# Kernel optimization log

Measured on AMD Instinct MI355X. Metric: run time of the kernel, lower is better.

## Reference

```python
import jax, jax.numpy as jnp
import numpy as np

N_EMBD = 1024
HEADS = 16
HEAD_DIM = N_EMBD // HEADS


def setup_inputs() -> dict:
    key = jax.random.key(0)
    k1, k2 = jax.random.split(key)
    x = jax.random.normal(k1, (2, 2048, N_EMBD), dtype=jnp.float32)
    W_qkv = jax.random.normal(k2, (N_EMBD, 3 * N_EMBD), dtype=jnp.float32) * (N_EMBD ** -0.5)
    b_qkv = jnp.zeros((3 * N_EMBD,), dtype=jnp.float32)
    return {"x": x, "W_qkv": W_qkv, "b_qkv": b_qkv}


def reference(x, W_qkv, b_qkv):
    B, T, _ = x.shape
    qkv = x @ W_qkv + b_qkv                      # [B, T, 3*n_embd]
    q, k, v = jnp.split(qkv, 3, axis=-1)
    q = q.reshape(B, T, HEADS, HEAD_DIM)
    k = k.reshape(B, T, HEADS, HEAD_DIM)
    v = v.reshape(B, T, HEADS, HEAD_DIM)
    attn = jnp.einsum('bthd,bThd->bhtT', q, k) / jnp.sqrt(jnp.float32(HEAD_DIM))
    causal = jnp.tril(jnp.ones((T, T), dtype=bool))  # [T, T]
    attn = jnp.where(causal, attn, -jnp.inf)
    attn = jax.nn.softmax(attn, axis=-1)
    # dropout is identity in deterministic/eval mode (training=False)
    out = jnp.einsum('bhtT,bThd->bthd', attn, v).reshape(B, T, N_EMBD)
    return out
```

## Files before the change

kernel.cpp:

```cpp
#include <hip/hip_runtime.h>
#include <hip/hip_bf16.h>

#define BATCH 2
#define TSEQ  2048
#define NEMBD 1024
#define HEADS 16
#define HDIM  64

typedef short          bf16x8 __attribute__((ext_vector_type(8)));
typedef float          f32x4  __attribute__((ext_vector_type(4)));
typedef unsigned short u16;

__device__ __forceinline__ u16 f2bf(float f) {
  unsigned int u = __float_as_uint(f);
  u += 0x7fffu + ((u >> 16) & 1u);
  return (u16)(u >> 16);
}

__device__ __forceinline__ void gld16(const u16* g, u16* l) {
  __builtin_amdgcn_global_load_lds(
      (const __attribute__((address_space(1))) unsigned int*)g,
      (__attribute__((address_space(3))) unsigned int*)l, 16, 0, 0);
}

__global__ __launch_bounds__(256) void k_prep(const float* __restrict__ x,
                                              u16* __restrict__ xb,
                                              const float* __restrict__ w,
                                              u16* __restrict__ wt) {
  __shared__ float tile[32][33];
  const int b = blockIdx.x;
  const int t = threadIdx.x;
  if (b < 4096) {
    int i = b * 256 + t;
    float4 v = ((const float4*)x)[i];
    ushort4 o;
    o.x = f2bf(v.x); o.y = f2bf(v.y); o.z = f2bf(v.z); o.w = f2bf(v.w);
    ((ushort4*)xb)[i] = o;
  } else {
    const int bt = b - 4096;
    const int n0 = (bt >> 5) * 32;
    const int k0 = (bt & 31) * 32;
    const int r  = t >> 3;
    const int c4 = (t & 7) * 4;
    float4 v = *(const float4*)(w + (size_t)(k0 + r) * 3072 + n0 + c4);
    tile[r][c4 + 0] = v.x; tile[r][c4 + 1] = v.y;
    tile[r][c4 + 2] = v.z; tile[r][c4 + 3] = v.w;
    __syncthreads();
    ushort4 o;
    o.x = f2bf(tile[c4 + 0][r]);
    o.y = f2bf(tile[c4 + 1][r]);
    o.z = f2bf(tile[c4 + 2][r]);
    o.w = f2bf(tile[c4 + 3][r]);
    *(ushort4*)(wt + (size_t)(n0 + r) * 1024 + k0 + c4) = o;
  }
}

__global__ __launch_bounds__(256, 3) void k_qkv_gemm(
    const u16* __restrict__ xb, const u16* __restrict__ wt,
    const float* __restrict__ bias,
    u16* __restrict__ qb, u16* __restrict__ kbuf, u16* __restrict__ vt) {
  __shared__ __align__(16) u16 As[128 * 64];
  __shared__ __align__(16) u16 Bs[128 * 64];

  const int t    = threadIdx.x;
  const int wv   = t >> 6;
  const int lane = t & 63;
  const int m    = lane & 15;
  const int quad = lane >> 4;
  const int lin  = blockIdx.x;
  const int cp   = lin >> 5;
  const int rp   = ((lin & 7) << 2) | ((lin >> 3) & 3);
  const int row0 = rp * 128;
  const int col0 = cp * 128;
  const int wr   = (wv >> 1) * 64;
  const int wc   = (wv & 1) * 64;

  const int sr = wv * 32 + (lane >> 3);
  const int gs = (lane & 7) ^ (sr & 7);
  const u16* ag = xb + (size_t)(row0 + sr) * 1024 + gs * 8;
  const u16* bg = wt + (size_t)(col0 + sr) * 1024 + gs * 8;
  u16* al = As + (wv * 32) * 64;
  u16* bl = Bs + (wv * 32) * 64;

  f32x4 acc[4][4];
  const f32x4 zf = {0.f, 0.f, 0.f, 0.f};
  for (int i = 0; i < 4; ++i)
    for (int j = 0; j < 4; ++j) acc[i][j] = zf;

  for (int kt = 0; kt < 16; ++kt) {
    const int kk = kt * 64;
    __syncthreads();
    gld16(ag + kk,             al);
    gld16(ag + kk +  8 * 1024, al +  8 * 64);
    gld16(ag + kk + 16 * 1024, al + 16 * 64);
    gld16(ag + kk + 24 * 1024, al + 24 * 64);
    gld16(bg + kk,             bl);
    gld16(bg + kk +  8 * 1024, bl +  8 * 64);
    gld16(bg + kk + 16 * 1024, bl + 16 * 64);
    gld16(bg + kk + 24 * 1024, bl + 24 * 64);
    __syncthreads();

#pragma unroll
    for (int h = 0; h < 2; ++h) {
      const int g = ((quad + 4 * h) ^ (m & 7)) * 8;
      bf16x8 af[4], bfr[4];
#pragma unroll
      for (int mt = 0; mt < 4; ++mt)
        af[mt] = *(const bf16x8*)(As + (wr + mt * 16 + m) * 64 + g);
#pragma unroll
      for (int nt = 0; nt < 4; ++nt)
        bfr[nt] = *(const bf16x8*)(Bs + (wc + nt * 16 + m) * 64 + g);
#pragma unroll
      for (int mt = 0; mt < 4; ++mt)
#pragma unroll
        for (int nt = 0; nt < 4; ++nt)
          acc[mt][nt] = __builtin_amdgcn_mfma_f32_16x16x32_bf16(
              af[mt], bfr[nt], acc[mt][nt], 0, 0, 0);
    }
  }

  const int sec = col0 >> 10;
#pragma unroll
  for (int nt = 0; nt < 4; ++nt) {
    const int Cc = col0 + wc + nt * 16 + m;
    const float bv = bias[Cc];
    const int c = Cc & 1023;
    const int h = c >> 6;
    const int d = c & 63;
#pragma unroll
    for (int mt = 0; mt < 4; ++mt) {
      const int Rbase = row0 + wr + mt * 16 + quad * 4;
      const int bb = Rbase >> 11;
      const int t0 = Rbase & 2047;
      const int bh = bb * HEADS + h;
      if (sec == 0) {
#pragma unroll
        for (int rg = 0; rg < 4; ++rg) {
          float v = (acc[mt][nt][rg] + bv) * 0.125f;
          qb[(size_t)(bh * TSEQ + t0 + rg) * HDIM + d] = f2bf(v);
        }
      } else if (sec == 1) {
#pragma unroll
        for (int rg = 0; rg < 4; ++rg) {
          float v = acc[mt][nt][rg] + bv;
          kbuf[(size_t)(bh * TSEQ + t0 + rg) * HDIM + d] = f2bf(v);
        }
      } else {
        ushort4 pk;
        pk.x = f2bf(acc[mt][nt][0] + bv);
        pk.y = f2bf(acc[mt][nt][1] + bv);
        pk.z = f2bf(acc[mt][nt][2] + bv);
        pk.w = f2bf(acc[mt][nt][3] + bv);
        *(ushort4*)(vt + (size_t)(bh * HDIM + d) * TSEQ + t0) = pk;
      }
    }
  }
}

__global__ __launch_bounds__(256, 3) void k_attn(
    const u16* __restrict__ qb, const u16* __restrict__ kbuf,
    const u16* __restrict__ vt, float* __restrict__ out) {
  __shared__ __align__(16) u16 Kb[2][4096];
  __shared__ __align__(16) u16 Vb[2][4096];
  __shared__ __align__(16) u16 pt[4][16 * 72];

  const int t     = threadIdx.x;
  const int wv    = t >> 6;
  const int lane  = t & 63;
  const int m     = lane & 15;
  const int quad  = lane >> 4;
  const int bh    = blockIdx.x & 31;
  const int qtg   = 31 - (blockIdx.x >> 5);
  const int qbase = (qtg * 4 + wv) * 16;
  const int nkt   = qtg + 1;

  u16* pw = &pt[wv][0];

  const u16* qrow = qb + ((size_t)bh * TSEQ + qbase + m) * HDIM + quad * 8;
  bf16x8 aq0 = *(const bf16x8*)(qrow);
  bf16x8 aq1 = *(const bf16x8*)(qrow + 32);

  const int sr = wv * 16 + (lane >> 3);
  const int gs = (lane & 7) ^ (sr & 7);
  const u16* kg = kbuf + ((size_t)bh * TSEQ + sr) * HDIM + gs * 8;
  const u16* vg = vt + ((size_t)bh * HDIM + sr) * TSEQ + gs * 8;
  u16* klds = &Kb[0][wv * 16 * 64];
  u16* vlds = &Vb[0][wv * 16 * 64];

  const int swL = (quad ^ (m & 7)) * 8;
  const int swH = ((quad + 4) ^ (m & 7)) * 8;

  f32x4 o[4];
  const f32x4 zf = {0.f, 0.f, 0.f, 0.f};
  for (int nt = 0; nt < 4; ++nt) o[nt] = zf;
  float rsum = 0.f;
  const int qi = qbase + m;

  gld16(kg,             klds);
  gld16(kg + 8 * HDIM,  klds + 8 * 64);
  gld16(vg,             vlds);
  gld16(vg + 8 * TSEQ,  vlds + 8 * 64);
  __syncthreads();

  for (int kt = 0; kt < nkt; ++kt) {
    const int b = kt & 1;
    const u16* kb0 = &Kb[b][0];
    const u16* vb0 = &Vb[b][0];

    f32x4 s[4];
    for (int nt = 0; nt < 4; ++nt) s[nt] = zf;
#pragma unroll
    for (int nt = 0; nt < 4; ++nt) {
      bf16x8 kf = *(const bf16x8*)(kb0 + (nt * 16 + m) * 64 + swL);
      s[nt] = __builtin_amdgcn_mfma_f32_16x16x32_bf16(kf, aq0, s[nt], 0, 0, 0);
    }
#pragma unroll
    for (int nt = 0; nt < 4; ++nt) {
      bf16x8 kf = *(const bf16x8*)(kb0 + (nt * 16 + m) * 64 + swH);
      s[nt] = __builtin_amdgcn_mfma_f32_16x16x32_bf16(kf, aq1, s[nt], 0, 0, 0);
    }

    bf16x8 vfL[4], vfH[4];
#pragma unroll
    for (int nt = 0; nt < 4; ++nt) {
      vfL[nt] = *(const bf16x8*)(vb0 + (nt * 16 + m) * 64 + swL);
      vfH[nt] = *(const bf16x8*)(vb0 + (nt * 16 + m) * 64 + swH);
    }

    if (kt + 1 < nkt) {
      const int nb = (kt + 1) & 1;
      const u16* kgn = kg + (size_t)(kt + 1) * 64 * HDIM;
      const u16* vgn = vg + (kt + 1) * 64;
      u16* kl = &Kb[nb][wv * 16 * 64];
      u16* vl = &Vb[nb][wv * 16 * 64];
      gld16(kgn,            kl);
      gld16(kgn + 8 * HDIM, kl + 8 * 64);
      gld16(vgn,            vl);
      gld16(vgn + 8 * TSEQ, vl + 8 * 64);
    }

    if (kt == nkt - 1) {
      const int kb = kt * 64 + quad * 4;
#pragma unroll
      for (int nt = 0; nt < 4; ++nt)
#pragma unroll
        for (int rg = 0; rg < 4; ++rg)
          if (kb + nt * 16 + rg > qi) s[nt][rg] = -1e30f;
    }

#pragma unroll
    for (int nt = 0; nt < 4; ++nt) {
      float p0 = __expf(s[nt][0]), p1 = __expf(s[nt][1]);
      float p2 = __expf(s[nt][2]), p3 = __expf(s[nt][3]);
      rsum += (p0 + p1) + (p2 + p3);
      ushort4 pk = {f2bf(p0), f2bf(p1), f2bf(p2), f2bf(p3)};
      *(ushort4*)(pw + m * 72 + nt * 16 + quad * 4) = pk;
    }
    bf16x8 bp0 = *(const bf16x8*)(pw + m * 72 + quad * 8);
    bf16x8 bp1 = *(const bf16x8*)(pw + m * 72 + 32 + quad * 8);

#pragma unroll
    for (int nt = 0; nt < 4; ++nt)
      o[nt] = __builtin_amdgcn_mfma_f32_16x16x32_bf16(vfL[nt], bp0, o[nt], 0, 0, 0);
#pragma unroll
    for (int nt = 0; nt < 4; ++nt)
      o[nt] = __builtin_amdgcn_mfma_f32_16x16x32_bf16(vfH[nt], bp1, o[nt], 0, 0, 0);

    __syncthreads();
  }

  rsum += __shfl_xor(rsum, 16);
  rsum += __shfl_xor(rsum, 32);
  const float inv = 1.0f / rsum;

  const int bb = bh >> 4;
  const int h  = bh & 15;
  float* ob = out + ((size_t)(bb * TSEQ + qi) * NEMBD + h * HDIM + quad * 4);
#pragma unroll
  for (int nt = 0; nt < 4; ++nt) {
    float4 st;
    st.x = o[nt][0] * inv; st.y = o[nt][1] * inv;
    st.z = o[nt][2] * inv; st.w = o[nt][3] * inv;
    *(float4*)(ob + nt * 16) = st;
  }
}

extern "C" void kernel_launch(void* const* d_in, const int* in_sizes, int n_in,
                              void* d_out, int out_size, void* d_ws, size_t ws_size,
                              hipStream_t stream) {
  (void)in_sizes; (void)n_in; (void)out_size; (void)ws_size;
  const float* x    = (const float*)d_in[0];
  const float* W    = (const float*)d_in[1];
  const float* bqkv = (const float*)d_in[2];
  float* out = (float*)d_out;

  u16* ws   = (u16*)d_ws;
  u16* qb   = ws;
  u16* kbuf = ws + 4194304;
  u16* vt   = ws + 2 * 4194304;
  u16* xb   = ws + 3 * 4194304;
  u16* wt   = ws + 4 * 4194304;

  hipLaunchKernelGGL(k_prep, dim3(7168), dim3(256), 0, stream, x, xb, W, wt);
  hipLaunchKernelGGL(k_qkv_gemm, dim3(768), dim3(256), 0, stream,
                     xb, wt, bqkv, qb, kbuf, vt);
  hipLaunchKernelGGL(k_attn, dim3(1024), dim3(256), 0, stream,
                     qb, kbuf, vt, out);
}
```

Baseline: 140.5 us.

## Restructure QKV GEMM into double-buffered 256x256 tiles with interleaved loads

The QKV projection GEMM moves from 128x128 tiles with 256 threads to 256x256 tiles with 512 threads. LDS is now double-buffered, and the next k-slice's global-to-LDS loads are split into quarters interleaved with MFMA quadrants, using explicit vmcnt waits, barriers and s_setprio. The goal is to hide load latency behind compute and raise operand reuse per LDS byte. In exchange the grid shrinks to 192 blocks using 128KB of LDS each, which may leave some compute units idle.

```diff
diff --git a/kernel.cpp b/kernel.cpp
--- a/kernel.cpp
+++ b/kernel.cpp
@@ -22,6 +22,9 @@
       (const __attribute__((address_space(1))) unsigned int*)g,
       (__attribute__((address_space(3))) unsigned int*)l, 16, 0, 0);
 }
+
+#define BARSB() do { __builtin_amdgcn_s_barrier();      \
+                     __builtin_amdgcn_sched_barrier(0); } while (0)
 
 __global__ __launch_bounds__(256) void k_prep(const float* __restrict__ x,
                                               u16* __restrict__ xb,
@@ -55,81 +58,145 @@
   }
 }
 
-__global__ __launch_bounds__(256, 3) void k_qkv_gemm(
+__global__ __launch_bounds__(512, 2) void k_qkv_gemm(
     const u16* __restrict__ xb, const u16* __restrict__ wt,
     const float* __restrict__ bias,
     u16* __restrict__ qb, u16* __restrict__ kbuf, u16* __restrict__ vt) {
-  __shared__ __align__(16) u16 As[128 * 64];
-  __shared__ __align__(16) u16 Bs[128 * 64];
+  __shared__ __align__(16) u16 Ab[2][256 * 64];
+  __shared__ __align__(16) u16 Bb[2][256 * 64];
 
   const int t    = threadIdx.x;
-  const int wv   = t >> 6;
+  const int wid  = t >> 6;
   const int lane = t & 63;
   const int m    = lane & 15;
   const int quad = lane >> 4;
-  const int lin  = blockIdx.x;
-  const int cp   = lin >> 5;
-  const int rp   = ((lin & 7) << 2) | ((lin >> 3) & 3);
-  const int row0 = rp * 128;
-  const int col0 = cp * 128;
-  const int wr   = (wv >> 1) * 64;
-  const int wc   = (wv & 1) * 64;
-
-  const int sr = wv * 32 + (lane >> 3);
-  const int gs = (lane & 7) ^ (sr & 7);
-  const u16* ag = xb + (size_t)(row0 + sr) * 1024 + gs * 8;
-  const u16* bg = wt + (size_t)(col0 + sr) * 1024 + gs * 8;
-  u16* al = As + (wv * 32) * 64;
-  u16* bl = Bs + (wv * 32) * 64;
-
-  f32x4 acc[4][4];
+  const int wm   = wid >> 2;
+  const int wn   = wid & 3;
+
+  const int rp   = blockIdx.x & 15;
+  const int cp   = blockIdx.x >> 4;
+  const int row0 = rp * 256;
+  const int col0 = cp * 256;
+
+  const int trA = t >> 3;
+  const int gs  = (t & 7) ^ (trA & 7);
+  const int rB0 = ((t >> 8) & 1) * 64 + (trA & 31);
+  const u16* agp = xb + (size_t)(row0 + trA) * 1024 + gs * 8;
+  const u16* bgp = wt + (size_t)(col0 + rB0) * 1024 + gs * 8;
+  const int ldsArow = wid * 8;
+  const int ldsBrow = (wid >> 2) * 64 + (wid & 3) * 8;
+
+  const int sw0 = (quad ^ (m & 7)) * 8;
+  const int sw1 = ((4 + quad) ^ (m & 7)) * 8;
+
+  f32x4 acc[8][4];
   const f32x4 zf = {0.f, 0.f, 0.f, 0.f};
-  for (int i = 0; i < 4; ++i)
+#pragma unroll
+  for (int i = 0; i < 8; ++i)
+#pragma unroll
     for (int j = 0; j < 4; ++j) acc[i][j] = zf;
 
-  for (int kt = 0; kt < 16; ++kt) {
-    const int kk = kt * 64;
-    __syncthreads();
-    gld16(ag + kk,             al);
-    gld16(ag + kk +  8 * 1024, al +  8 * 64);
-    gld16(ag + kk + 16 * 1024, al + 16 * 64);
-    gld16(ag + kk + 24 * 1024, al + 24 * 64);
-    gld16(bg + kk,             bl);
-    gld16(bg + kk +  8 * 1024, bl +  8 * 64);
-    gld16(bg + kk + 16 * 1024, bl + 16 * 64);
-    gld16(bg + kk + 24 * 1024, bl + 24 * 64);
-    __syncthreads();
-
-#pragma unroll
-    for (int h = 0; h < 2; ++h) {
-      const int g = ((quad + 4 * h) ^ (m & 7)) * 8;
-      bf16x8 af[4], bfr[4];
-#pragma unroll
-      for (int mt = 0; mt < 4; ++mt)
-        af[mt] = *(const bf16x8*)(As + (wr + mt * 16 + m) * 64 + g);
-#pragma unroll
-      for (int nt = 0; nt < 4; ++nt)
-        bfr[nt] = *(const bf16x8*)(Bs + (wc + nt * 16 + m) * 64 + g);
-#pragma unroll
-      for (int mt = 0; mt < 4; ++mt)
-#pragma unroll
-        for (int nt = 0; nt < 4; ++nt)
-          acc[mt][nt] = __builtin_amdgcn_mfma_f32_16x16x32_bf16(
-              af[mt], bfr[nt], acc[mt][nt], 0, 0, 0);
-    }
+  gld16(agp,          &Ab[0][(  0 + ldsArow) * 64]);
+  gld16(agp + 131072, &Ab[0][(128 + ldsArow) * 64]);
+  gld16(agp +  65536, &Ab[0][( 64 + ldsArow) * 64]);
+  gld16(agp + 196608, &Ab[0][(192 + ldsArow) * 64]);
+  gld16(bgp,          &Bb[0][(  0 + ldsBrow) * 64]);
+  gld16(bgp + 131072, &Bb[0][(128 + ldsBrow) * 64]);
+  gld16(bgp +  32768, &Bb[0][( 32 + ldsBrow) * 64]);
+  gld16(bgp + 163840, &Bb[0][(160 + ldsBrow) * 64]);
+  asm volatile("s_waitcnt vmcnt(0)" ::: "memory");
+  BARSB();
+
+  bf16x8 a[4][2], b0[2][2], b1[2][2];
+
+#define RD_A(H)                                                         \
+  _Pragma("unroll") for (int mf = 0; mf < 4; ++mf) {                    \
+    const u16* r_ = cA + (wm * 128 + (H) * 64 + mf * 16 + m) * 64;      \
+    a[mf][0] = *(const bf16x8*)(r_ + sw0);                              \
+    a[mf][1] = *(const bf16x8*)(r_ + sw1);                              \
+  }
+#define RD_B(H, BR)                                                     \
+  _Pragma("unroll") for (int nf = 0; nf < 2; ++nf) {                    \
+    const u16* r_ = cB + (wn * 64 + (H) * 32 + nf * 16 + m) * 64;       \
+    BR[nf][0] = *(const bf16x8*)(r_ + sw0);                             \
+    BR[nf][1] = *(const bf16x8*)(r_ + sw1);                             \
+  }
+#define MFMA_Q(MB, NB, BR)                                              \
+  __builtin_amdgcn_s_setprio(1);                                        \
+  _Pragma("unroll") for (int mf = 0; mf < 4; ++mf)                      \
+    _Pragma("unroll") for (int nf = 0; nf < 2; ++nf) {                  \
+      acc[(MB) + mf][(NB) + nf] = __builtin_amdgcn_mfma_f32_16x16x32_bf16( \
+          a[mf][0], BR[nf][0], acc[(MB) + mf][(NB) + nf], 0, 0, 0);     \
+      acc[(MB) + mf][(NB) + nf] = __builtin_amdgcn_mfma_f32_16x16x32_bf16( \
+          a[mf][1], BR[nf][1], acc[(MB) + mf][(NB) + nf], 0, 0, 0);     \
+    }                                                                   \
+  __builtin_amdgcn_s_setprio(0);
+
+  for (int kt = 0; kt < 15; ++kt) {
+    const u16* cA = &Ab[kt & 1][0];
+    const u16* cB = &Bb[kt & 1][0];
+    u16* nA = &Ab[(kt + 1) & 1][0];
+    u16* nB = &Bb[(kt + 1) & 1][0];
+    const int kn = (kt + 1) * 64;
+
+    RD_A(0)
+    RD_B(0, b0)
+    gld16(agp + kn,          nA + (  0 + ldsArow) * 64);
+    gld16(agp + kn + 131072, nA + (128 + ldsArow) * 64);
+    BARSB();
+    MFMA_Q(0, 0, b0)
+    asm volatile("s_waitcnt vmcnt(2)" ::: "memory");
+    BARSB();
+
+    RD_B(1, b1)
+    gld16(bgp + kn,          nB + (  0 + ldsBrow) * 64);
+    gld16(bgp + kn + 131072, nB + (128 + ldsBrow) * 64);
+    BARSB();
+    MFMA_Q(0, 2, b1)
+    BARSB();
+
+    RD_A(1)
+    gld16(agp + kn +  65536, nA + ( 64 + ldsArow) * 64);
+    gld16(agp + kn + 196608, nA + (192 + ldsArow) * 64);
+    BARSB();
+    MFMA_Q(4, 2, b1)
+    BARSB();
+
+    gld16(bgp + kn +  32768, nB + ( 32 + ldsBrow) * 64);
+    gld16(bgp + kn + 163840, nB + (160 + ldsBrow) * 64);
+    BARSB();
+    MFMA_Q(4, 0, b0)
+    asm volatile("s_waitcnt vmcnt(4)" ::: "memory");
+    BARSB();
+  }
+
+  asm volatile("s_waitcnt vmcnt(0)" ::: "memory");
+  __builtin_amdgcn_s_barrier();
+  __builtin_amdgcn_sched_barrier(0);
+  {
+    const u16* cA = &Ab[1][0];
+    const u16* cB = &Bb[1][0];
+    RD_A(0)
+    RD_B(0, b0)
+    RD_B(1, b1)
+    MFMA_Q(0, 0, b0)
+    MFMA_Q(0, 2, b1)
+    RD_A(1)
+    MFMA_Q(4, 2, b1)
+    MFMA_Q(4, 0, b0)
   }
 
   const int sec = col0 >> 10;
 #pragma unroll
   for (int nt = 0; nt < 4; ++nt) {
-    const int Cc = col0 + wc + nt * 16 + m;
+    const int Cc = col0 + wn * 64 + nt * 16 + m;
     const float bv = bias[Cc];
     const int c = Cc & 1023;
     const int h = c >> 6;
     const int d = c & 63;
 #pragma unroll
-    for (int mt = 0; mt < 4; ++mt) {
-      const int Rbase = row0 + wr + mt * 16 + quad * 4;
+    for (int mt = 0; mt < 8; ++mt) {
+      const int Rbase = row0 + wm * 128 + mt * 16 + quad * 4;
       const int bb = Rbase >> 11;
       const int t0 = Rbase & 2047;
       const int bh = bb * HEADS + h;
@@ -155,6 +222,9 @@
       }
     }
   }
+#undef RD_A
+#undef RD_B
+#undef MFMA_Q
 }
 
 __global__ __launch_bounds__(256, 3) void k_attn(
@@ -181,9 +251,9 @@
   bf16x8 aq1 = *(const bf16x8*)(qrow + 32);
 
   const int sr = wv * 16 + (lane >> 3);
-  const int gs = (lane & 7) ^ (sr & 7);
-  const u16* kg = kbuf + ((size_t)bh * TSEQ + sr) * HDIM + gs * 8;
-  const u16* vg = vt + ((size_t)bh * HDIM + sr) * TSEQ + gs * 8;
+  const int gsk = (lane & 7) ^ (sr & 7);
+  const u16* kg = kbuf + ((size_t)bh * TSEQ + sr) * HDIM + gsk * 8;
+  const u16* vg = vt + ((size_t)bh * HDIM + sr) * TSEQ + gsk * 8;
   u16* klds = &Kb[0][wv * 16 * 64];
   u16* vlds = &Vb[0][wv * 16 * 64];
 
@@ -302,7 +372,7 @@
   u16* wt   = ws + 4 * 4194304;
 
   hipLaunchKernelGGL(k_prep, dim3(7168), dim3(256), 0, stream, x, xb, W, wt);
-  hipLaunchKernelGGL(k_qkv_gemm, dim3(768), dim3(256), 0, stream,
+  hipLaunchKernelGGL(k_qkv_gemm, dim3(192), dim3(512), 0, stream,
                      xb, wt, bqkv, qb, kbuf, vt);
   hipLaunchKernelGGL(k_attn, dim3(1024), dim3(256), 0, stream,
                      qb, kbuf, vt, out);
```

New measurement: 146.3 us. +4.2%, slower.
